# Kernel optimization log

Hardware: AMD Instinct MI355X
Metric: run time of the kernel (lower is better)

Reference implementation:

```python
import jax, jax.numpy as jnp
import numpy as np

# Architecture constants (match init_kwargs)
B = 64          # batch
INPUT = 128     # input_size
SS = 9          # simple_size (V1 kernel)
DIMS = INPUT - SS + 1            # 120, V1 output grid
SN = 8          # simple_number (orientations)
PS = 4          # phis_sfs (phases)
C = SN * PS     # 32 V1 channels
V4K = 8         # v4_size
V4S = 4         # v4_stride
V4D = (DIMS - V4K) // V4S + 1    # 29
ORI = 16        # v4_orientation_number


def _patches(x, k, s):
    """x: [N, H, W] -> [N, oh, ow, k*k]; kernel dim is row-major (kh, kw),
    matching torch .unfold(2,k,s).unfold(3,k,s).view(..., k*k)."""
    p = jax.lax.conv_general_dilated_patches(x[:, None], (k, k), (s, s), 'VALID')
    return jnp.moveaxis(p, 1, -1)  # [N, oh, ow, k*k]


def setup_inputs() -> dict:
    key = jax.random.key(0)
    k0, k1, k2, k3 = jax.random.split(key, 4)
    x = jax.random.normal(k0, (B, 1, INPUT, INPUT), jnp.float32)
    # Unshared (per-location) V1 weights: [C, dims, dims, ss^2]
    simple_weight = jax.random.normal(k1, (C, DIMS, DIMS, SS * SS), jnp.float32) * 0.05
    # Unshared V4 pooling weights: [ORI, SN, v4d, v4d, v4k^2]
    v4_weight = jax.random.normal(k2, (ORI, SN, V4D, V4D, V4K * V4K), jnp.float32) * 0.05
    dec_w = jax.random.normal(k3, (2, ORI * V4D * V4D), jnp.float32) * 0.01
    dec_b = jnp.zeros((2,), jnp.float32)
    return {"x": x, "simple_weight": simple_weight, "v4_weight": v4_weight,
            "dec_w": dec_w, "dec_b": dec_b}


def reference(x, simple_weight, v4_weight, dec_w, dec_b):
    b = x.shape[0]
    # --- V1 locally-connected layer (unfold + per-location weighted sum) ---
    p1 = _patches(x[:, 0], SS, 1)                         # [B, 120, 120, 81]
    v1 = jnp.einsum('bijk,cijk->bcij', p1, simple_weight)  # [B, 32, 120, 120]
    # --- complex-cell pooling over phases (relu then combine phis_sfs) ---
    cplx = jax.nn.relu(v1).reshape(b, SN, PS, DIMS, DIMS).mean(2)  # [B, 8, 120, 120]
    # --- V4 locally-connected pooling per orientation channel ---
    p2 = _patches(cplx.reshape(b * SN, DIMS, DIMS), V4K, V4S)
    p2 = p2.reshape(b, SN, V4D, V4D, V4K * V4K)            # [B, 8, 29, 29, 64]
    v4 = jnp.einsum('bsijk,osijk->boij', p2, v4_weight)    # [B, 16, 29, 29]
    # --- decision readout ---
    flat = v4.reshape(b, -1)                               # [B, 13456]
    return flat @ dec_w.T + dec_b                          # [B, 2]
```

## Files before the change

kernel.cpp:

```cpp
#include <hip/hip_runtime.h>
#include <hip/hip_bf16.h>
#include <stdint.h>

#define B64   64
#define DIMS  120
#define NLOC  (DIMS*DIMS)
#define V4D   29
#define NLOC4 (V4D*V4D)

typedef __attribute__((ext_vector_type(8))) short bf16x8;
typedef __attribute__((ext_vector_type(4))) float f32x4;

__device__ __forceinline__ unsigned short f2bf(float f) {
    unsigned u = __float_as_uint(f);
    u += 0x7fffu + ((u >> 16) & 1u);
    return (unsigned short)(u >> 16);
}

__device__ __forceinline__ void gload16(const float* g, float* l) {
    __builtin_amdgcn_global_load_lds(
        (const __attribute__((address_space(1))) unsigned int*)g,
        (__attribute__((address_space(3))) unsigned int*)l, 16, 0, 0);
}

__global__ __launch_bounds__(256) void k0_pack(const float* __restrict__ x,
                                               unsigned short* __restrict__ xrep,
                                               unsigned short* __restrict__ xrepT) {
    __shared__ unsigned short tile[16 * 16 * 64];
    int blk = blockIdx.x;
    int isT = (blk >= 128) ? 1 : 0;
    int b2 = blk - 128 * isT;
    int g = b2 >> 3;
    int fb = (b2 & 7) << 4;
    int tid = threadIdx.x;
    int bb = tid >> 2, c4 = (tid & 3) << 2;
#pragma unroll 4
    for (int rr = 0; rr < 16; ++rr) {
        int row, col;
        if (!isT) { row = 8 * g + rr; col = fb + c4; }
        else      { row = fb + rr;    col = 8 * g + c4; }
        f32x4 v;
        if (row < 128 && col < 128)
            v = *(const f32x4*)(x + ((size_t)bb * 128 + row) * 128 + col);
        else
            v = (f32x4){0.f, 0.f, 0.f, 0.f};
#pragma unroll
        for (int cc = 0; cc < 4; ++cc) {
            int d1 = isT ? rr : (c4 + cc);
            int d2 = isT ? (c4 + cc) : rr;
            tile[(d1 * 16 + d2) * 64 + bb] = f2bf(v[cc]);
        }
    }
    __syncthreads();
    unsigned short* outp = isT ? xrepT : xrep;
    int b = tid & 63;
#pragma unroll
    for (int it = 0; it < 32; ++it) {
        int u = (it * 256 + tid) >> 6;
        int d1 = u & 15, rq = u >> 4;
        bf16x8 pk;
#pragma unroll
        for (int q = 0; q < 8; ++q)
            pk[q] = (short)tile[(d1 * 16 + rq + q) * 64 + b];
        size_t off = ((((size_t)rq * 128 + (fb + d1)) * 16 + g) * 64 + b) * 8;
        *(bf16x8*)(outp + off) = pk;
    }
}

__global__ __launch_bounds__(256) void k1_v1(const unsigned short* __restrict__ xrep,
                                             const unsigned short* __restrict__ xrepT,
                                             const float* __restrict__ sw,
                                             unsigned short* __restrict__ cplx) {
    __shared__ __align__(16) char smraw[41472];
    float* stagef = (float*)smraw;
    float* pool2 = (float*)smraw;

    int tid = threadIdx.x;
    int blk = blockIdx.x;
    int blk2 = (blk & 7) * 450 + (blk >> 3);
    int loc0 = blk2 * 4;

    int w = tid >> 6, l = tid & 63;

#pragma unroll
    for (int cc = 0; cc < 8; ++cc) {
        int c = w * 8 + cc;
        const float* g = sw + ((size_t)c * NLOC + loc0) * 81;
        float* lp = stagef + c * 324;
        gload16(g + l * 4, lp + l * 4);
        if (l < 17)
            gload16(g + 256 + l * 4, lp + 256 + l * 4);
    }

    int loc = loc0 + w;
    int i = loc / DIMS, j = loc - i * DIMS;
    int ln = l & 15, t = l >> 4;
    int r = i & 7, g2 = i >> 3, rc = j & 7, gc = j >> 3;

    const float* bb0 = stagef + (size_t)ln * 324 + w * 81;
    const float* bb1 = bb0 + 16 * 324;
    int off2 = (t == 0) ? 8 : ((t == 1) ? 72 : 80);
    int strd2 = (t == 0) ? 9 : ((t == 1) ? 1 : 0);
    bool keep0 = (t <= 2);
    bool keepR = (t <= 1);

    f32x4 acc[4][2];
#pragma unroll
    for (int mt = 0; mt < 4; ++mt)
#pragma unroll
        for (int nt = 0; nt < 2; ++nt)
            acc[mt][nt] = (f32x4){0.f, 0.f, 0.f, 0.f};

    __syncthreads();

#pragma unroll
    for (int ks = 0; ks < 3; ++ks) {
        int ch = ks * 4 + t;
        const unsigned short* abase;
        if (ks < 2) {
            int col = j + ch;
            abase = xrep + (((size_t)r * 128 + col) * 16 + g2) * 512;
        } else {
            const unsigned short* a0 = xrep + (((size_t)r * 128 + (j + 8)) * 16 + g2) * 512;
            int gc2 = gc + ((t >= 2) ? 1 : 0);
            const unsigned short* a1 = xrepT + (((size_t)rc * 128 + (i + 8)) * 16 + gc2) * 512;
            abase = (t == 0) ? a0 : a1;
        }
        bf16x8 a[4];
#pragma unroll
        for (int mt = 0; mt < 4; ++mt)
            a[mt] = *(const bf16x8*)(abase + (size_t)(ln + 16 * mt) * 8);
        bf16x8 bfr[2];
        if (ks < 2) {
#pragma unroll
            for (int jj = 0; jj < 8; ++jj) {
                bfr[0][jj] = (short)f2bf(bb0[ch + jj * 9]);
                bfr[1][jj] = (short)f2bf(bb1[ch + jj * 9]);
            }
        } else {
            {
                float v0 = bb0[off2], v1 = bb1[off2];
                bfr[0][0] = (short)f2bf(keep0 ? v0 : 0.0f);
                bfr[1][0] = (short)f2bf(keep0 ? v1 : 0.0f);
            }
            int o = off2;
#pragma unroll
            for (int jj = 1; jj < 8; ++jj) {
                o += strd2;
                float v0 = bb0[o], v1 = bb1[o];
                bfr[0][jj] = (short)f2bf(keepR ? v0 : 0.0f);
                bfr[1][jj] = (short)f2bf(keepR ? v1 : 0.0f);
            }
        }
#pragma unroll
        for (int mt = 0; mt < 4; ++mt)
#pragma unroll
            for (int nt = 0; nt < 2; ++nt)
                acc[mt][nt] = __builtin_amdgcn_mfma_f32_16x16x32_bf16(
                    a[mt], bfr[nt], acc[mt][nt], 0, 0, 0);
    }

    __syncthreads();
    float* pl = pool2 + w * 64 * 9;
#pragma unroll
    for (int mt = 0; mt < 4; ++mt)
#pragma unroll
        for (int nt = 0; nt < 2; ++nt)
#pragma unroll
            for (int reg = 0; reg < 4; ++reg) {
                float v = fmaxf(acc[mt][nt][reg], 0.0f);
                v += __shfl_xor(v, 1, 64);
                v += __shfl_xor(v, 2, 64);
                if ((ln & 3) == 0) {
                    int b = 16 * mt + 4 * t + reg;
                    int s = 4 * nt + (ln >> 2);
                    pl[b * 9 + s] = v * 0.25f;
                }
            }
    __syncthreads();
    bf16x8 po;
#pragma unroll
    for (int s = 0; s < 8; ++s)
        po[s] = (short)f2bf(pl[l * 9 + s]);
    *(bf16x8*)(cplx + (size_t)loc * 512 + l * 8) = po;
}

__global__ __launch_bounds__(256) void k2_v4(const unsigned short* __restrict__ cplx,
                                             const float* __restrict__ vw,
                                             float* __restrict__ v4s) {
    __shared__ __align__(16) char smraw[128 * 68 * 4];
    float* stg = (float*)smraw;
    float* pool = (float*)smraw;

    int tid = threadIdx.x;
    int blk = blockIdx.x;
    int loc = (blk < 840) ? ((blk & 7) * 105 + (blk >> 3)) : 840;
    int oi = loc / V4D, oj = loc - oi * V4D;

    int w = tid >> 6, l = tid & 63;

    if (l < 16) {
#pragma unroll
        for (int m = 0; m < 32; ++m) {
            int ro = w * 32 + m;
            int o = ro >> 3, s = ro & 7;
            const float* g = vw + ((size_t)ro * NLOC4 + loc) * 64;
            float* lp = stg + (s * 16 + o) * 68;
            gload16(g + l * 4, lp + l * 4);
        }
    }

    int ln = l & 15, t = l >> 4;
    f32x4 acc[4];
#pragma unroll
    for (int mt = 0; mt < 4; ++mt) acc[mt] = (f32x4){0.f, 0.f, 0.f, 0.f};

    __syncthreads();

    const float* brow = stg + ln * 68;
#pragma unroll
    for (int kk = 0; kk < 4; ++kk) {
        int pos = 4 * (w * 4 + kk) + t;
        int kh = pos >> 3, kw = pos & 7;
        int iloc = (oi * 4 + kh) * DIMS + oj * 4 + kw;
        const unsigned short* ab = cplx + (size_t)iloc * 512 + ln * 8;
        bf16x8 a[4];
#pragma unroll
        for (int mt = 0; mt < 4; ++mt)
            a[mt] = *(const bf16x8*)(ab + mt * 128);
        bf16x8 bb;
#pragma unroll
        for (int s = 0; s < 8; ++s)
            bb[s] = (short)f2bf(brow[s * 16 * 68 + pos]);
#pragma unroll
        for (int mt = 0; mt < 4; ++mt)
            acc[mt] = __builtin_amdgcn_mfma_f32_16x16x32_bf16(a[mt], bb, acc[mt], 0, 0, 0);
    }
    __syncthreads();
#pragma unroll
    for (int mt = 0; mt < 4; ++mt)
#pragma unroll
        for (int reg = 0; reg < 4; ++reg)
            pool[((w * 64) + 16 * mt + 4 * t + reg) * 16 + ln] = acc[mt][reg];
    __syncthreads();
    int o = tid & 15, brw = tid >> 4;
#pragma unroll
    for (int itb = 0; itb < 4; ++itb) {
        int b = brw + 16 * itb;
        float s = pool[(0 * 64 + b) * 16 + o] + pool[(1 * 64 + b) * 16 + o] +
                  pool[(2 * 64 + b) * 16 + o] + pool[(3 * 64 + b) * 16 + o];
        v4s[(size_t)loc * 1024 + b * 16 + o] = s;
    }
}

__global__ __launch_bounds__(256) void k3_dec(const float* __restrict__ v4s,
                                              const float* __restrict__ dw,
                                              const float* __restrict__ db,
                                              float* __restrict__ out) {
    int b = blockIdx.x, tid = threadIdx.x;
    float a0 = 0.f, a1 = 0.f;
    for (int loc = tid; loc < NLOC4; loc += 256) {
        const float* vp = v4s + (size_t)loc * 1024 + b * 16;
#pragma unroll
        for (int o4 = 0; o4 < 4; ++o4) {
            f32x4 v = *(const f32x4*)(vp + o4 * 4);
#pragma unroll
            for (int q = 0; q < 4; ++q) {
                int o = o4 * 4 + q;
                a0 += v[q] * dw[o * NLOC4 + loc];
                a1 += v[q] * dw[16 * NLOC4 + o * NLOC4 + loc];
            }
        }
    }
    __shared__ float r0[256], r1[256];
    r0[tid] = a0; r1[tid] = a1;
    __syncthreads();
    for (int s = 128; s > 0; s >>= 1) {
        if (tid < s) { r0[tid] += r0[tid + s]; r1[tid] += r1[tid + s]; }
        __syncthreads();
    }
    if (tid == 0) {
        out[2 * b + 0] = r0[0] + db[0];
        out[2 * b + 1] = r1[0] + db[1];
    }
}

extern "C" void kernel_launch(void* const* d_in, const int* in_sizes, int n_in,
                              void* d_out, int out_size, void* d_ws, size_t ws_size,
                              hipStream_t stream) {
    const float* x  = (const float*)d_in[0];
    const float* sw = (const float*)d_in[1];
    const float* vw = (const float*)d_in[2];
    const float* dw = (const float*)d_in[3];
    const float* db = (const float*)d_in[4];
    float* out = (float*)d_out;

    char* ws = (char*)d_ws;
    unsigned short* xrep  = (unsigned short*)ws;
    unsigned short* xrepT = (unsigned short*)(ws + 16777216);
    unsigned short* cplx  = (unsigned short*)(ws + 33554432);
    float*          v4s   = (float*)(ws + 48300032);

    k0_pack<<<256, 256, 0, stream>>>(x, xrep, xrepT);
    k1_v1<<<NLOC / 4, 256, 0, stream>>>(xrep, xrepT, sw, cplx);
    k2_v4<<<NLOC4, 256, 0, stream>>>(cplx, vw, v4s);
    k3_dec<<<B64, 256, 0, stream>>>(v4s, dw, db, out);
}
```

Measured before the change: 286.3 us.

## Fuse decision readout into V4 kernel with shuffle reduction and atomics

Removes the separate readout kernel and the v4s intermediate buffer. Each V4 block multiplies its pooled outputs by the matching readout weights, reduces across orientations with wave shuffles, and atomically adds per-batch partials into the output, which the pack kernel pre-initialises with the bias. This drops one launch and the v4s write/read round trip. In exchange it adds 841×128 float atomics on only 128 addresses, and the summation order becomes nondeterministic.

```diff
diff --git a/kernel.cpp b/kernel.cpp
--- a/kernel.cpp
+++ b/kernel.cpp
@@ -25,14 +25,17 @@
 
 __global__ __launch_bounds__(256) void k0_pack(const float* __restrict__ x,
                                                unsigned short* __restrict__ xrep,
-                                               unsigned short* __restrict__ xrepT) {
+                                               unsigned short* __restrict__ xrepT,
+                                               const float* __restrict__ db,
+                                               float* __restrict__ out) {
     __shared__ unsigned short tile[16 * 16 * 64];
     int blk = blockIdx.x;
+    int tid = threadIdx.x;
+    if (blk == 0 && tid < 128) out[tid] = db[tid & 1];
     int isT = (blk >= 128) ? 1 : 0;
     int b2 = blk - 128 * isT;
     int g = b2 >> 3;
     int fb = (b2 & 7) << 4;
-    int tid = threadIdx.x;
     int bb = tid >> 2, c4 = (tid & 3) << 2;
 #pragma unroll 4
     for (int rr = 0; rr < 16; ++rr) {
@@ -187,7 +190,8 @@
 
 __global__ __launch_bounds__(256) void k2_v4(const unsigned short* __restrict__ cplx,
                                              const float* __restrict__ vw,
-                                             float* __restrict__ v4s) {
+                                             const float* __restrict__ dw,
+                                             float* __restrict__ out) {
     __shared__ __align__(16) char smraw[128 * 68 * 4];
     float* stg = (float*)smraw;
     float* pool = (float*)smraw;
@@ -244,44 +248,24 @@
             pool[((w * 64) + 16 * mt + 4 * t + reg) * 16 + ln] = acc[mt][reg];
     __syncthreads();
     int o = tid & 15, brw = tid >> 4;
+    const float* dw0 = dw + (size_t)o * NLOC4 + loc;
+    float w0 = dw0[0];
+    float w1 = dw0[16 * NLOC4];
 #pragma unroll
     for (int itb = 0; itb < 4; ++itb) {
         int b = brw + 16 * itb;
         float s = pool[(0 * 64 + b) * 16 + o] + pool[(1 * 64 + b) * 16 + o] +
                   pool[(2 * 64 + b) * 16 + o] + pool[(3 * 64 + b) * 16 + o];
-        v4s[(size_t)loc * 1024 + b * 16 + o] = s;
-    }
-}
-
-__global__ __launch_bounds__(256) void k3_dec(const float* __restrict__ v4s,
-                                              const float* __restrict__ dw,
-                                              const float* __restrict__ db,
-                                              float* __restrict__ out) {
-    int b = blockIdx.x, tid = threadIdx.x;
-    float a0 = 0.f, a1 = 0.f;
-    for (int loc = tid; loc < NLOC4; loc += 256) {
-        const float* vp = v4s + (size_t)loc * 1024 + b * 16;
-#pragma unroll
-        for (int o4 = 0; o4 < 4; ++o4) {
-            f32x4 v = *(const f32x4*)(vp + o4 * 4);
-#pragma unroll
-            for (int q = 0; q < 4; ++q) {
-                int o = o4 * 4 + q;
-                a0 += v[q] * dw[o * NLOC4 + loc];
-                a1 += v[q] * dw[16 * NLOC4 + o * NLOC4 + loc];
-            }
-        }
-    }
-    __shared__ float r0[256], r1[256];
-    r0[tid] = a0; r1[tid] = a1;
-    __syncthreads();
-    for (int s = 128; s > 0; s >>= 1) {
-        if (tid < s) { r0[tid] += r0[tid + s]; r1[tid] += r1[tid + s]; }
-        __syncthreads();
-    }
-    if (tid == 0) {
-        out[2 * b + 0] = r0[0] + db[0];
-        out[2 * b + 1] = r1[0] + db[1];
+        float c0 = s * w0;
+        float c1 = s * w1;
+        c0 += __shfl_xor(c0, 1, 64);  c1 += __shfl_xor(c1, 1, 64);
+        c0 += __shfl_xor(c0, 2, 64);  c1 += __shfl_xor(c1, 2, 64);
+        c0 += __shfl_xor(c0, 4, 64);  c1 += __shfl_xor(c1, 4, 64);
+        c0 += __shfl_xor(c0, 8, 64);  c1 += __shfl_xor(c1, 8, 64);
+        if (o == 0) {
+            atomicAdd(out + 2 * b + 0, c0);
+            atomicAdd(out + 2 * b + 1, c1);
+        }
     }
 }
 
@@ -299,10 +283,8 @@
     unsigned short* xrep  = (unsigned short*)ws;
     unsigned short* xrepT = (unsigned short*)(ws + 16777216);
     unsigned short* cplx  = (unsigned short*)(ws + 33554432);
-    float*          v4s   = (float*)(ws + 48300032);
-
-    k0_pack<<<256, 256, 0, stream>>>(x, xrep, xrepT);
+
+    k0_pack<<<256, 256, 0, stream>>>(x, xrep, xrepT, db, out);
     k1_v1<<<NLOC / 4, 256, 0, stream>>>(xrep, xrepT, sw, cplx);
-    k2_v4<<<NLOC4, 256, 0, stream>>>(cplx, vw, v4s);
-    k3_dec<<<B64, 256, 0, stream>>>(v4s, dw, db, out);
-}
+    k2_v4<<<NLOC4, 256, 0, stream>>>(cplx, vw, dw, out);
+}
```

After: 353.5 us. 23.5% more time.

## Use one-wave V1 blocks per location and split decision readout with atomics

Applied to the files above, without the earlier changes.

The V1 kernel now runs one 64-thread block per spatial location, staging only that location's 32x81 weights into LDS. It hoists all A-fragment global loads ahead of the barrier so they overlap the weight staging. The decision kernel is split into four partial blocks per batch element that combine results with atomicAdd, and the bias is written earlier by the pack kernel. This aims for more parallelism and better latency hiding, at the cost of more blocks, per-block overhead and non-deterministic float summation order.

```diff
diff --git a/kernel.cpp b/kernel.cpp
--- a/kernel.cpp
+++ b/kernel.cpp
@@ -22,17 +22,25 @@
         (const __attribute__((address_space(1))) unsigned int*)g,
         (__attribute__((address_space(3))) unsigned int*)l, 16, 0, 0);
 }
+__device__ __forceinline__ void gload4(const float* g, float* l) {
+    __builtin_amdgcn_global_load_lds(
+        (const __attribute__((address_space(1))) unsigned int*)g,
+        (__attribute__((address_space(3))) unsigned int*)l, 4, 0, 0);
+}
 
 __global__ __launch_bounds__(256) void k0_pack(const float* __restrict__ x,
                                                unsigned short* __restrict__ xrep,
-                                               unsigned short* __restrict__ xrepT) {
+                                               unsigned short* __restrict__ xrepT,
+                                               const float* __restrict__ db,
+                                               float* __restrict__ out) {
     __shared__ unsigned short tile[16 * 16 * 64];
     int blk = blockIdx.x;
+    int tid = threadIdx.x;
+    if (blk == 0 && tid < 128) out[tid] = db[tid & 1];
     int isT = (blk >= 128) ? 1 : 0;
     int b2 = blk - 128 * isT;
     int g = b2 >> 3;
     int fb = (b2 & 7) << 4;
-    int tid = threadIdx.x;
     int bb = tid >> 2, c4 = (tid & 3) << 2;
 #pragma unroll 4
     for (int rr = 0; rr < 16; ++rr) {
@@ -67,58 +75,38 @@
     }
 }
 
-__global__ __launch_bounds__(256) void k1_v1(const unsigned short* __restrict__ xrep,
-                                             const unsigned short* __restrict__ xrepT,
-                                             const float* __restrict__ sw,
-                                             unsigned short* __restrict__ cplx) {
-    __shared__ __align__(16) char smraw[41472];
-    float* stagef = (float*)smraw;
-    float* pool2 = (float*)smraw;
-
-    int tid = threadIdx.x;
+__global__ __launch_bounds__(64, 3) void k1_v1(const unsigned short* __restrict__ xrep,
+                                               const unsigned short* __restrict__ xrepT,
+                                               const float* __restrict__ sw,
+                                               unsigned short* __restrict__ cplx) {
+    __shared__ __align__(16) float stg[32 * 84];
+    __shared__ float pool[64 * 9];
+
+    int l = threadIdx.x;
     int blk = blockIdx.x;
-    int blk2 = (blk & 7) * 450 + (blk >> 3);
-    int loc0 = blk2 * 4;
-
-    int w = tid >> 6, l = tid & 63;
-
-#pragma unroll
-    for (int cc = 0; cc < 8; ++cc) {
-        int c = w * 8 + cc;
-        const float* g = sw + ((size_t)c * NLOC + loc0) * 81;
-        float* lp = stagef + c * 324;
-        gload16(g + l * 4, lp + l * 4);
-        if (l < 17)
-            gload16(g + 256 + l * 4, lp + 256 + l * 4);
-    }
-
-    int loc = loc0 + w;
+    int loc = (blk & 7) * 1800 + (blk >> 3);
     int i = loc / DIMS, j = loc - i * DIMS;
+
+    bool lastLoc = (loc == NLOC - 1);
+#pragma unroll
+    for (int c = 0; c < 32; ++c) {
+        const float* g = sw + ((size_t)c * NLOC + loc) * 81;
+        float* lp = stg + c * 84;
+        int nl = (c == 31) ? (lastLoc ? 20 : 21) : 21;
+        if (l < nl) gload16(g + l * 4, lp + l * 4);
+    }
+    if (lastLoc && l == 0)
+        gload4(sw + ((size_t)31 * NLOC + loc) * 81 + 80, stg + 31 * 84 + 80);
+
     int ln = l & 15, t = l >> 4;
     int r = i & 7, g2 = i >> 3, rc = j & 7, gc = j >> 3;
 
-    const float* bb0 = stagef + (size_t)ln * 324 + w * 81;
-    const float* bb1 = bb0 + 16 * 324;
-    int off2 = (t == 0) ? 8 : ((t == 1) ? 72 : 80);
-    int strd2 = (t == 0) ? 9 : ((t == 1) ? 1 : 0);
-    bool keep0 = (t <= 2);
-    bool keepR = (t <= 1);
-
-    f32x4 acc[4][2];
-#pragma unroll
-    for (int mt = 0; mt < 4; ++mt)
-#pragma unroll
-        for (int nt = 0; nt < 2; ++nt)
-            acc[mt][nt] = (f32x4){0.f, 0.f, 0.f, 0.f};
-
-    __syncthreads();
-
+    bf16x8 a[3][4];
 #pragma unroll
     for (int ks = 0; ks < 3; ++ks) {
-        int ch = ks * 4 + t;
         const unsigned short* abase;
         if (ks < 2) {
-            int col = j + ch;
+            int col = j + ks * 4 + t;
             abase = xrep + (((size_t)r * 128 + col) * 16 + g2) * 512;
         } else {
             const unsigned short* a0 = xrep + (((size_t)r * 128 + (j + 8)) * 16 + g2) * 512;
@@ -126,10 +114,30 @@
             const unsigned short* a1 = xrepT + (((size_t)rc * 128 + (i + 8)) * 16 + gc2) * 512;
             abase = (t == 0) ? a0 : a1;
         }
-        bf16x8 a[4];
 #pragma unroll
         for (int mt = 0; mt < 4; ++mt)
-            a[mt] = *(const bf16x8*)(abase + (size_t)(ln + 16 * mt) * 8);
+            a[ks][mt] = *(const bf16x8*)(abase + (size_t)(ln + 16 * mt) * 8);
+    }
+
+    const float* bb0 = stg + (size_t)ln * 84;
+    const float* bb1 = stg + (size_t)(16 + ln) * 84;
+    int off2 = (t == 0) ? 8 : ((t == 1) ? 72 : 80);
+    int strd2 = (t == 0) ? 9 : ((t == 1) ? 1 : 0);
+    bool keep0 = (t <= 2);
+    bool keepR = (t <= 1);
+
+    f32x4 acc[4][2];
+#pragma unroll
+    for (int mt = 0; mt < 4; ++mt)
+#pragma unroll
+        for (int nt = 0; nt < 2; ++nt)
+            acc[mt][nt] = (f32x4){0.f, 0.f, 0.f, 0.f};
+
+    __syncthreads();
+
+#pragma unroll
+    for (int ks = 0; ks < 3; ++ks) {
+        int ch = ks * 4 + t;
         bf16x8 bfr[2];
         if (ks < 2) {
 #pragma unroll
@@ -157,11 +165,9 @@
 #pragma unroll
             for (int nt = 0; nt < 2; ++nt)
                 acc[mt][nt] = __builtin_amdgcn_mfma_f32_16x16x32_bf16(
-                    a[mt], bfr[nt], acc[mt][nt], 0, 0, 0);
-    }
-
-    __syncthreads();
-    float* pl = pool2 + w * 64 * 9;
+                    a[ks][mt], bfr[nt], acc[mt][nt], 0, 0, 0);
+    }
+
 #pragma unroll
     for (int mt = 0; mt < 4; ++mt)
 #pragma unroll
@@ -174,14 +180,15 @@
                 if ((ln & 3) == 0) {
                     int b = 16 * mt + 4 * t + reg;
                     int s = 4 * nt + (ln >> 2);
-                    pl[b * 9 + s] = v * 0.25f;
+                    pool[b * 9 + s] = v * 0.25f;
                 }
             }
     __syncthreads();
+
     bf16x8 po;
 #pragma unroll
     for (int s = 0; s < 8; ++s)
-        po[s] = (short)f2bf(pl[l * 9 + s]);
+        po[s] = (short)f2bf(pool[l * 9 + s]);
     *(bf16x8*)(cplx + (size_t)loc * 512 + l * 8) = po;
 }
 
@@ -255,11 +262,14 @@
 
 __global__ __launch_bounds__(256) void k3_dec(const float* __restrict__ v4s,
                                               const float* __restrict__ dw,
-                                              const float* __restrict__ db,
                                               float* __restrict__ out) {
-    int b = blockIdx.x, tid = threadIdx.x;
+    int blk = blockIdx.x, tid = threadIdx.x;
+    int b = blk >> 2, part = blk & 3;
+    int start = part * 210;
+    int lim = start + ((part == 3) ? 211 : 210);
+    int loc = start + tid;
     float a0 = 0.f, a1 = 0.f;
-    for (int loc = tid; loc < NLOC4; loc += 256) {
+    if (loc < lim) {
         const float* vp = v4s + (size_t)loc * 1024 + b * 16;
 #pragma unroll
         for (int o4 = 0; o4 < 4; ++o4) {
@@ -280,8 +290,8 @@
         __syncthreads();
     }
     if (tid == 0) {
-        out[2 * b + 0] = r0[0] + db[0];
-        out[2 * b + 1] = r1[0] + db[1];
+        atomicAdd(out + 2 * b + 0, r0[0]);
+        atomicAdd(out + 2 * b + 1, r1[0]);
     }
 }
 
@@ -301,8 +311,8 @@
     unsigned short* cplx  = (unsigned short*)(ws + 33554432);
     float*          v4s   = (float*)(ws + 48300032);
 
-    k0_pack<<<256, 256, 0, stream>>>(x, xrep, xrepT);
-    k1_v1<<<NLOC / 4, 256, 0, stream>>>(xrep, xrepT, sw, cplx);
+    k0_pack<<<256, 256, 0, stream>>>(x, xrep, xrepT, db, out);
+    k1_v1<<<NLOC, 64, 0, stream>>>(xrep, xrepT, sw, cplx);
     k2_v4<<<NLOC4, 256, 0, stream>>>(cplx, vw, v4s);
-    k3_dec<<<B64, 256, 0, stream>>>(v4s, dw, db, out);
-}
+    k3_dec<<<4 * B64, 256, 0, stream>>>(v4s, dw, out);
+}
```

Result: faster. 273.0 us (-4.6%).
